# Performance work log

Hardware: AMD Instinct MI355X
Metric: run time of the kernel (lower is better)

The kernel has to match this reference:

```python
import jax, jax.numpy as jnp
import numpy as np

B, C, F, H, W = 8, 16, 256, 112, 112   # batch, cells/image, channels, height, width
NB = 3                                  # tgt_shape = (3, 3) adaptive pool bins


def setup_inputs() -> dict:
    key = jax.random.key(0)
    kf, ky, kx, kry, krx, kn = jax.random.split(key, 6)
    feature_maps = jax.random.normal(kf, (B, F, H, W), jnp.float32)
    N = B * C
    # random rectangular cell blobs with bernoulli interior holes + guaranteed core
    cy = jax.random.randint(ky, (N, 1, 1), 20, H - 20)
    cx = jax.random.randint(kx, (N, 1, 1), 20, W - 20)
    ry = jax.random.randint(kry, (N, 1, 1), 5, 18)
    rx = jax.random.randint(krx, (N, 1, 1), 5, 18)
    yy = jnp.arange(H)[None, :, None]
    xx = jnp.arange(W)[None, None, :]
    rect = (jnp.abs(yy - cy) <= ry) & (jnp.abs(xx - cx) <= rx)
    noise = jax.random.bernoulli(kn, 0.8, (N, H, W))
    core = (jnp.abs(yy - cy) <= 2) & (jnp.abs(xx - cx) <= 2)
    cell_masks = rect & (noise | core)            # [N, H, W] bool, each nonempty
    cell_counts = jnp.full((B,), C, jnp.int32)    # fixed cells per image
    return {"feature_maps": feature_maps, "cell_masks": cell_masks,
            "cell_counts": cell_counts}


def _bin_membership(lo, hi, length):
    # adaptive-pool bin i covers [lo + floor(i*sz/NB), lo + ceil((i+1)*sz/NB))
    i = jnp.arange(NB)
    sz = (hi - lo)[..., None]                      # [B, C, 1]
    start = lo[..., None] + (i * sz) // NB         # [B, C, NB]
    end = lo[..., None] + ((i + 1) * sz + NB - 1) // NB
    pos = jnp.arange(length)
    return (pos >= start[..., None]) & (pos < end[..., None])  # [B, C, NB, L]


def reference(feature_maps, cell_masks, cell_counts):
    Bv, Fv, Hv, Wv = feature_maps.shape
    Cv = cell_masks.shape[0] // Bv
    masks = cell_masks.reshape(Bv, Cv, Hv, Wv)
    # tight bbox per cell (first/last True row and column, exclusive end)
    rows = masks.any(-1)                            # [B, C, H]
    cols = masks.any(-2)                            # [B, C, W]
    y0 = jnp.argmax(rows, -1)
    y1 = Hv - jnp.argmax(rows[..., ::-1], -1)
    x0 = jnp.argmax(cols, -1)
    x1 = Wv - jnp.argmax(cols[..., ::-1], -1)
    ymem = _bin_membership(y0, y1, Hv)              # [B, C, NB, H]
    xmem = _bin_membership(x0, x1, Wv)              # [B, C, NB, W]
    neg = jnp.finfo(feature_maps.dtype).min
    feat = feature_maps[:, None]                    # [B, 1, F, H, W]
    m = masks[:, :, None]                           # [B, C, 1, H, W]
    pooled = []
    for i in range(NB):
        ym = ymem[:, :, i][:, :, None, :, None]     # [B, C, 1, H, 1]
        for j in range(NB):
            xm = xmem[:, :, j][:, :, None, None, :]  # [B, C, 1, 1, W]
            inbin = ym & xm
            # inside bin & mask -> feature; inside bin & ~mask -> 0 (zeroed crop);
            # outside bin -> -inf (excluded from max)
            v = jnp.where(inbin & m, feat, jnp.where(inbin, 0.0, neg))
            pooled.append(v.max((-1, -2)))          # [B, C, F]
    out = jnp.stack(pooled, -1)                     # [B, C, F, 9], index = i*NB + j
    # matches torch pooled.view(-1): flatten order f*9 + i*3 + j
    return out.reshape(Bv * Cv, Fv * NB * NB)
```

## Files before the change

### kernel.cpp

```cpp
#include <hip/hip_runtime.h>
#include <float.h>

#define B_  8
#define C_  16
#define N_  (B_*C_)
#define F_  256
#define H_  112
#define W_  112
#define HW_ (H_*W_)
#define NB_ 3

#define RB_STRIDE 40
#define NPACK 14
#define FSTRIP 8


__global__ __launch_bounds__(256) void bbox_kernel(const int4* __restrict__ mask4,
                                                   int* __restrict__ bb,
                                                   unsigned long long* __restrict__ rowbits) {
    int n = blockIdx.x, t = threadIdx.x;
    const int4* m = mask4 + (size_t)n * (HW_ / 4);
    int ymin = 1 << 20, ymax = -1, xmin = 1 << 20, xmax = -1;
    for (int i = t; i < HW_ / 4; i += 256) {
        int4 v = m[i];
        int y = i / 28;
        int xb = (i - y * 28) * 4;
        if (v.x | v.y | v.z | v.w) { ymin = min(ymin, y); ymax = max(ymax, y); }
        if (v.x) { xmin = min(xmin, xb);     xmax = max(xmax, xb);     }
        if (v.y) { xmin = min(xmin, xb + 1); xmax = max(xmax, xb + 1); }
        if (v.z) { xmin = min(xmin, xb + 2); xmax = max(xmax, xb + 2); }
        if (v.w) { xmin = min(xmin, xb + 3); xmax = max(xmax, xb + 3); }
    }
    #pragma unroll
    for (int off = 32; off; off >>= 1) {
        ymin = min(ymin, __shfl_xor(ymin, off));
        ymax = max(ymax, __shfl_xor(ymax, off));
        xmin = min(xmin, __shfl_xor(xmin, off));
        xmax = max(xmax, __shfl_xor(xmax, off));
    }
    __shared__ int red[4][4];
    __shared__ int sb[3];
    int wave = t >> 6;
    if ((t & 63) == 0) {
        red[wave][0] = ymin; red[wave][1] = ymax;
        red[wave][2] = xmin; red[wave][3] = xmax;
    }
    __syncthreads();
    if (t == 0) {
        for (int w = 1; w < 4; ++w) {
            ymin = min(ymin, red[w][0]); ymax = max(ymax, red[w][1]);
            xmin = min(xmin, red[w][2]); xmax = max(xmax, red[w][3]);
        }
        int y0 = ymin, y1 = ymax + 1, x0 = xmin, x1 = xmax + 1;
        int* o = bb + n * 16;
        o[0] = y0; o[1] = y1; o[2] = x0; o[3] = x1;
        int szy = y1 - y0, szx = x1 - x0;
        for (int i = 0; i < NB_; ++i) {
            o[4+i]  = y0 + (i*szy)/NB_;
            o[7+i]  = y0 + ((i+1)*szy + NB_-1)/NB_;
            o[10+i] = x0 + (i*szx)/NB_;
            o[13+i] = x0 + ((i+1)*szx + NB_-1)/NB_;
        }
        sb[0] = y0; sb[1] = szy; sb[2] = x0 & ~3;
    }
    __syncthreads();
    {
        int y0 = sb[0], bh = sb[1], x0a = sb[2];
        int lane = t & 63;
        const int* mrow = (const int*)mask4 + (size_t)n * HW_ + x0a + lane;
        for (int dy = wave; dy < bh; dy += 4) {
            int v = mrow[(size_t)(y0 + dy) * W_];
            unsigned long long bits = __ballot(v != 0);
            if (lane == 0) rowbits[n * RB_STRIDE + dy] = bits;
        }
    }
}

__global__ __launch_bounds__(256, 4) void pool_kernel(
        const float* __restrict__ feat,
        const unsigned long long* __restrict__ rowbits,
        const int* __restrict__ bb, float* __restrict__ out) {
    int tid  = threadIdx.x;
    int lane = tid & 63, w = tid >> 6;
    int gw = blockIdx.x * 4 + w;
    int n  = gw >> 5;
    int f0 = (gw & 31) * FSTRIP;
    int b  = n >> 4;

    const int* o = bb + n * 16;
    int y0 = o[0], x0 = o[2];
    int bw = o[3] - x0;
    int x0a = x0 & ~3;
    int wbw = (x0 - x0a) + bw;

    int xq = lane & 15, rg = lane >> 4;
    int bi = min(rg, 2);
    int xq4 = (4 * xq < wbw) ? 4 * xq : 0;
    const float* gp = feat + (size_t)(b * F_ + f0) * HW_ + (size_t)y0 * W_ + x0a + xq4;

    int ysb  = o[4 + bi];
    int yeb1 = o[7 + bi] - 1;

    int roff[NPACK];
    #pragma unroll
    for (int u = 0; u < NPACK; ++u)
        roff[u] = (min(ysb + u, yeb1) - y0) * W_;

    unsigned long long mynib = 0;
    {
        const unsigned long long* rbp = rowbits + n * RB_STRIDE;
        #pragma unroll
        for (int u = 0; u < NPACK; ++u) {
            int dy = min(ysb + u, yeb1) - y0;
            mynib |= ((rbp[dy] >> (4 * xq)) & 0xFull) << (4 * u);
        }
    }

    int xg = x0a + 4 * xq;
    float lim[3][4];
    #pragma unroll
    for (int j = 0; j < 3; ++j) {
        int xs = o[10 + j], xe = o[13 + j];
        #pragma unroll
        for (int s = 0; s < 4; ++s) {
            int xx = xg + s;
            lim[j][s] = (xx >= xs && xx < xe) ? FLT_MAX : -FLT_MAX;
        }
    }

    for (int ff = 0; ff < FSTRIP; ++ff) {
        float4 cr[NPACK];
        #pragma unroll
        for (int u = 0; u < NPACK; ++u)
            cr[u] = *(const float4*)(gp + roff[u]);

        float a0 = -FLT_MAX, a1 = -FLT_MAX, a2 = -FLT_MAX, a3 = -FLT_MAX;
        #pragma unroll
        for (int u = 0; u < NPACK; ++u) {
            unsigned int nib = (unsigned int)(mynib >> (4 * u)) & 0xFu;
            a0 = fmaxf(a0, (nib & 1u) ? cr[u].x : 0.f);
            a1 = fmaxf(a1, (nib & 2u) ? cr[u].y : 0.f);
            a2 = fmaxf(a2, (nib & 4u) ? cr[u].z : 0.f);
            a3 = fmaxf(a3, (nib & 8u) ? cr[u].w : 0.f);
        }

        float part[3];
        #pragma unroll
        for (int j = 0; j < 3; ++j) {
            float r;
            r = fminf(a0, lim[j][0]);
            r = fmaxf(r, fminf(a1, lim[j][1]));
            r = fmaxf(r, fminf(a2, lim[j][2]));
            r = fmaxf(r, fminf(a3, lim[j][3]));
            part[j] = r;
        }
        #pragma unroll
        for (int off = 1; off <= 8; off <<= 1) {
            #pragma unroll
            for (int j = 0; j < 3; ++j)
                part[j] = fmaxf(part[j], __shfl_xor(part[j], off));
        }
        if (xq == 0 && rg < 3) {
            float* op = out + (size_t)(n * F_ + f0 + ff) * 9 + rg * 3;
            op[0] = part[0]; op[1] = part[1]; op[2] = part[2];
        }
        gp += HW_;
    }
}

extern "C" void kernel_launch(void* const* d_in, const int* in_sizes, int n_in,
                              void* d_out, int out_size, void* d_ws, size_t ws_size,
                              hipStream_t stream) {
    const float* feat = (const float*)d_in[0];
    const int*   mask = (const int*)d_in[1];
    int* bb = (int*)d_ws;
    unsigned long long* rowbits = (unsigned long long*)((char*)d_ws + 8192);

    bbox_kernel<<<N_, 256, 0, stream>>>((const int4*)mask, bb, rowbits);
    pool_kernel<<<1024, 256, 0, stream>>>(feat, rowbits, bb, (float*)d_out);
}
```

Baseline: 169.1 us.

## Double-buffer feature row loads and double channels per wave in pool kernel

```diff
diff --git a/kernel.cpp b/kernel.cpp
--- a/kernel.cpp
+++ b/kernel.cpp
@@ -12,7 +12,7 @@
 
 #define RB_STRIDE 40
 #define NPACK 14
-#define FSTRIP 8
+#define FSTRIP 16
 
 
 __global__ __launch_bounds__(256) void bbox_kernel(const int4* __restrict__ mask4,
@@ -76,15 +76,15 @@
     }
 }
 
-__global__ __launch_bounds__(256, 4) void pool_kernel(
+__global__ __launch_bounds__(256, 2) void pool_kernel(
         const float* __restrict__ feat,
         const unsigned long long* __restrict__ rowbits,
         const int* __restrict__ bb, float* __restrict__ out) {
     int tid  = threadIdx.x;
     int lane = tid & 63, w = tid >> 6;
     int gw = blockIdx.x * 4 + w;
-    int n  = gw >> 5;
-    int f0 = (gw & 31) * FSTRIP;
+    int n  = gw >> 4;
+    int f0 = (gw & 15) * FSTRIP;
     int b  = n >> 4;
 
     const int* o = bb + n * 16;
@@ -128,44 +128,54 @@
         }
     }
 
-    for (int ff = 0; ff < FSTRIP; ++ff) {
-        float4 cr[NPACK];
-        #pragma unroll
-        for (int u = 0; u < NPACK; ++u)
-            cr[u] = *(const float4*)(gp + roff[u]);
+    #define ISSUE(CR, P)                                                      \
+        { const float* _fp = gp + (size_t)(P) * HW_;                          \
+          _Pragma("unroll")                                                   \
+          for (int u = 0; u < NPACK; ++u)                                     \
+              CR[u] = *(const float4*)(_fp + roff[u]); }
 
-        float a0 = -FLT_MAX, a1 = -FLT_MAX, a2 = -FLT_MAX, a3 = -FLT_MAX;
-        #pragma unroll
-        for (int u = 0; u < NPACK; ++u) {
-            unsigned int nib = (unsigned int)(mynib >> (4 * u)) & 0xFu;
-            a0 = fmaxf(a0, (nib & 1u) ? cr[u].x : 0.f);
-            a1 = fmaxf(a1, (nib & 2u) ? cr[u].y : 0.f);
-            a2 = fmaxf(a2, (nib & 4u) ? cr[u].z : 0.f);
-            a3 = fmaxf(a3, (nib & 8u) ? cr[u].w : 0.f);
-        }
+    #define CONSUME(CR, P)                                                    \
+        { float a0 = -FLT_MAX, a1 = -FLT_MAX, a2 = -FLT_MAX, a3 = -FLT_MAX;   \
+          _Pragma("unroll")                                                   \
+          for (int u = 0; u < NPACK; ++u) {                                   \
+              unsigned int nib = (unsigned int)(mynib >> (4 * u)) & 0xFu;     \
+              a0 = fmaxf(a0, (nib & 1u) ? CR[u].x : 0.f);                     \
+              a1 = fmaxf(a1, (nib & 2u) ? CR[u].y : 0.f);                     \
+              a2 = fmaxf(a2, (nib & 4u) ? CR[u].z : 0.f);                     \
+              a3 = fmaxf(a3, (nib & 8u) ? CR[u].w : 0.f);                     \
+          }                                                                   \
+          float part[3];                                                      \
+          _Pragma("unroll")                                                   \
+          for (int j = 0; j < 3; ++j) {                                       \
+              float r;                                                        \
+              r = fminf(a0, lim[j][0]);                                       \
+              r = fmaxf(r, fminf(a1, lim[j][1]));                             \
+              r = fmaxf(r, fminf(a2, lim[j][2]));                             \
+              r = fmaxf(r, fminf(a3, lim[j][3]));                             \
+              part[j] = r;                                                    \
+          }                                                                   \
+          _Pragma("unroll")                                                   \
+          for (int off = 1; off <= 8; off <<= 1) {                            \
+              _Pragma("unroll")                                               \
+              for (int j = 0; j < 3; ++j)                                     \
+                  part[j] = fmaxf(part[j], __shfl_xor(part[j], off));         \
+          }                                                                   \
+          if (xq == 0 && rg < 3) {                                            \
+              float* op = out + (size_t)(n * F_ + f0 + (P)) * 9 + rg * 3;     \
+              op[0] = part[0]; op[1] = part[1]; op[2] = part[2];              \
+          } }
 
-        float part[3];
-        #pragma unroll
-        for (int j = 0; j < 3; ++j) {
-            float r;
-            r = fminf(a0, lim[j][0]);
-            r = fmaxf(r, fminf(a1, lim[j][1]));
-            r = fmaxf(r, fminf(a2, lim[j][2]));
-            r = fmaxf(r, fminf(a3, lim[j][3]));
-            part[j] = r;
-        }
-        #pragma unroll
-        for (int off = 1; off <= 8; off <<= 1) {
-            #pragma unroll
-            for (int j = 0; j < 3; ++j)
-                part[j] = fmaxf(part[j], __shfl_xor(part[j], off));
-        }
-        if (xq == 0 && rg < 3) {
-            float* op = out + (size_t)(n * F_ + f0 + ff) * 9 + rg * 3;
-            op[0] = part[0]; op[1] = part[1]; op[2] = part[2];
-        }
-        gp += HW_;
+    float4 crA[NPACK], crB[NPACK];
+    ISSUE(crA, 0);
+    ISSUE(crB, 1);
+    for (int p = 0; p < FSTRIP; p += 2) {
+        CONSUME(crA, p);
+        if (p + 2 < FSTRIP) ISSUE(crA, p + 2);
+        CONSUME(crB, p + 1);
+        if (p + 3 < FSTRIP) ISSUE(crB, p + 3);
     }
+    #undef ISSUE
+    #undef CONSUME
 }
 
 extern "C" void kernel_launch(void* const* d_in, const int* in_sizes, int n_in,
@@ -177,5 +187,5 @@
     unsigned long long* rowbits = (unsigned long long*)((char*)d_ws + 8192);
 
     bbox_kernel<<<N_, 256, 0, stream>>>((const int4*)mask, bb, rowbits);
-    pool_kernel<<<1024, 256, 0, stream>>>(feat, rowbits, bb, (float*)d_out);
+    pool_kernel<<<512, 256, 0, stream>>>(feat, rowbits, bb, (float*)d_out);
 }
```

After: 169.5 us. About the same (+0.2%).
